# Optimization experiments

Hardware: AMD Instinct MI355X
Metric: run time of the kernel (lower is better)

The kernel has to match this reference:

```python
import jax, jax.numpy as jnp
import numpy as np

B, S, D = 4, 2048, 512      # batch, seq_len, input_dim
E, H = 512, 8               # embed_dim, n_heads
HD = E // H                 # head_dim
ALPHA = 1.0                 # LRSA temperature


def setup_inputs() -> dict:
    key = jax.random.key(0)
    kx, kw1, kw2 = jax.random.split(key, 3)
    # xavier_uniform bounds for the two Linear layers (bias init is 0, as in module)
    b_qkv = float(np.sqrt(6.0 / (D + 3 * E)))
    b_o = float(np.sqrt(6.0 / (E + E)))
    return {
        "x": jax.random.normal(kx, (B, S, D), dtype=jnp.float32),
        "Wqkv": jax.random.uniform(kw1, (3 * E, D), jnp.float32, -b_qkv, b_qkv),
        "bqkv": jnp.zeros((3 * E,), jnp.float32),
        "Wo": jax.random.uniform(kw2, (E, E), jnp.float32, -b_o, b_o),
        "bo": jnp.zeros((E,), jnp.float32),
    }


def reference(x, Wqkv, bqkv, Wo, bo):
    Bx, Sx, _ = x.shape
    # QKV projection: [B,S,3E] -> [B,S,H,3*HD] -> [B,H,S,3*HD]
    qkv = (x @ Wqkv.T + bqkv).reshape(Bx, Sx, H, 3 * HD).transpose(0, 2, 1, 3)
    q, k, v = jnp.split(qkv, 3, axis=-1)  # each [B,H,S,HD]

    # LRSA: pairwise squared L2 distance logits ||q_i - k_j||^2
    q_norm2 = jnp.sum(q * q, axis=-1, keepdims=True)        # [B,H,S,1]
    k_norm2 = jnp.sum(k * k, axis=-1)[..., None, :]         # [B,H,1,S]
    qk = jnp.einsum("bhqd,bhkd->bhqk", q, k)                # [B,H,S,S]
    logits = q_norm2 - 2.0 * qk + k_norm2

    # global normalizers: frobenius norm of q, max per-token L2 norm of x
    fro_q = jnp.sqrt(jnp.sum(q * q))
    inf_2_x = jnp.max(jnp.sqrt(jnp.sum(x * x, axis=-1)))
    logits = logits / fro_q / inf_2_x

    attention = jax.nn.softmax(-ALPHA * logits, axis=-1)    # [B,H,S,S]
    values = jnp.einsum("bhqk,bhkd->bhqd", attention, v)    # [B,H,S,HD]
    values = values.transpose(0, 2, 1, 3).reshape(Bx, Sx, E)
    return values @ Wo.T + bo
```

## Files before the change

kernel.cpp:

```cpp
#include <hip/hip_runtime.h>
#include <hip/hip_bf16.h>
#include <math.h>

#define B_ 4
#define S_ 2048
#define D_ 512
#define E_ 512
#define H_ 8
#define HD_ 64
#define ALPHA_ 1.0f
#define M_ (B_*S_)
#define LOG2E_ 1.44269504088896340736f

typedef __attribute__((ext_vector_type(8))) short bf16x8;
typedef __attribute__((ext_vector_type(4))) float f32x4;

__device__ inline unsigned short f2bf(float f) {
    union { __hip_bfloat16 h; unsigned short u; } cv;
    cv.h = __float2bfloat16(f);
    return cv.u;
}
__device__ inline unsigned pack2bf(float a, float b) {
    union { __hip_bfloat162 h; unsigned u; } cv;
    cv.h = __float22bfloat162_rn(make_float2(a, b));
    return cv.u;
}

__global__ __launch_bounds__(256) void prep(const float* __restrict__ x,
                                            const float* __restrict__ Wqkv,
                                            const float* __restrict__ Wo,
                                            unsigned short* __restrict__ xbf,
                                            unsigned short* __restrict__ Wqkvb,
                                            unsigned short* __restrict__ Wob,
                                            float* __restrict__ xmax) {
    const int t   = threadIdx.x;
    const int bid = blockIdx.x;
    if (bid < 2048) {
        __shared__ float red[4];
        const int wid = t >> 6, lane = t & 63;
        const int row = bid * 4 + wid;
        const float* xr = &x[(size_t)row * D_ + lane * 8];
        const float4 a = *(const float4*)xr;
        const float4 b = *(const float4*)(xr + 4);
        float ss = a.x*a.x + a.y*a.y + a.z*a.z + a.w*a.w
                 + b.x*b.x + b.y*b.y + b.z*b.z + b.w*b.w;
        uint4 o;
        o.x = pack2bf(a.x, a.y); o.y = pack2bf(a.z, a.w);
        o.z = pack2bf(b.x, b.y); o.w = pack2bf(b.z, b.w);
        *(uint4*)&xbf[(size_t)row * D_ + lane * 8] = o;
        #pragma unroll
        for (int off = 32; off; off >>= 1) ss += __shfl_xor(ss, off);
        if (lane == 0) red[wid] = ss;
        __syncthreads();
        if (t == 0)
            xmax[bid] = fmaxf(fmaxf(red[0], red[1]), fmaxf(red[2], red[3]));
    } else {
        const int i  = (bid - 2048) * 256 + t;
        const int nq = 3 * E_ * D_ / 8;
        const float* src; unsigned short* dst; int j;
        if (i < nq) { src = Wqkv; dst = Wqkvb; j = i; }
        else        { src = Wo;   dst = Wob;   j = i - nq; }
        const float4 a = *(const float4*)&src[(size_t)j * 8];
        const float4 b = *(const float4*)&src[(size_t)j * 8 + 4];
        uint4 o;
        o.x = pack2bf(a.x, a.y); o.y = pack2bf(a.z, a.w);
        o.z = pack2bf(b.x, b.y); o.w = pack2bf(b.z, b.w);
        *(uint4*)&dst[(size_t)j * 8] = o;
    }
}

template<int N, int MODE>
__global__ __launch_bounds__(256) void gemm_mfma(const unsigned short* __restrict__ Abf,
                                                 const unsigned short* __restrict__ Wbf,
                                                 const float* __restrict__ bias,
                                                 void* __restrict__ out0,
                                                 void* __restrict__ out1,
                                                 void* __restrict__ out2,
                                                 float* __restrict__ part,
                                                 float* __restrict__ kn2) {
    __shared__ __align__(16) char At[16384];
    __shared__ __align__(16) char Wt[16384];

    const int t  = threadIdx.x;
    const int w  = t >> 6;
    const int l  = t & 63;
    const int g  = l >> 4;
    const int c  = l & 15;
    const int wm = w >> 1;
    const int wn = w & 1;
    const int m0 = blockIdx.y * 128;
    const int n0 = blockIdx.x * 128;

    f32x4 acc[4][4];
    #pragma unroll
    for (int i = 0; i < 4; ++i)
        #pragma unroll
        for (int j = 0; j < 4; ++j)
            #pragma unroll
            for (int r = 0; r < 4; ++r) acc[i][j][r] = 0.f;

    for (int k0 = 0; k0 < 512; k0 += 64) {
        __syncthreads();
        #pragma unroll
        for (int i = 0; i < 4; ++i) {
            const int idx = t + i * 256;
            const int r   = idx >> 3;
            const int j   = idx & 7;
            const int dst = r * 128 + ((j * 16) ^ ((r & 7) << 4));
            *(uint4*)(At + dst) = *(const uint4*)&Abf[(size_t)(m0 + r) * 512 + k0 + j * 8];
            *(uint4*)(Wt + dst) = *(const uint4*)&Wbf[(size_t)(n0 + r) * 512 + k0 + j * 8];
        }
        __syncthreads();

        bf16x8 af[4][2], wf[4][2];
        #pragma unroll
        for (int mt = 0; mt < 4; ++mt) {
            const int row = wm * 64 + mt * 16 + c;
            const int sw  = (row & 7) << 4;
            #pragma unroll
            for (int kc = 0; kc < 2; ++kc)
                af[mt][kc] = *(const bf16x8*)(At + row * 128 + (((kc * 4 + g) * 16) ^ sw));
        }
        #pragma unroll
        for (int nt = 0; nt < 4; ++nt) {
            const int row = wn * 64 + nt * 16 + c;
            const int sw  = (row & 7) << 4;
            #pragma unroll
            for (int kc = 0; kc < 2; ++kc)
                wf[nt][kc] = *(const bf16x8*)(Wt + row * 128 + (((kc * 4 + g) * 16) ^ sw));
        }
        #pragma unroll
        for (int mt = 0; mt < 4; ++mt)
            #pragma unroll
            for (int nt = 0; nt < 4; ++nt) {
                acc[mt][nt] = __builtin_amdgcn_mfma_f32_16x16x32_bf16(af[mt][0], wf[nt][0], acc[mt][nt], 0, 0, 0);
                acc[mt][nt] = __builtin_amdgcn_mfma_f32_16x16x32_bf16(af[mt][1], wf[nt][1], acc[mt][nt], 0, 0, 0);
            }
    }

    if (MODE == 1) {
        #pragma unroll
        for (int mt = 0; mt < 4; ++mt)
            #pragma unroll
            for (int reg = 0; reg < 4; ++reg) {
                const int m = m0 + wm * 64 + mt * 16 + g * 4 + reg;
                #pragma unroll
                for (int nt = 0; nt < 4; ++nt) {
                    const int n = n0 + wn * 64 + nt * 16 + c;
                    ((float*)out0)[(size_t)m * N + n] = acc[mt][nt][reg] + bias[n];
                }
            }
        return;
    }

    const int hb  = 2 * blockIdx.x + wn;
    const int cls = hb % 3;
    const int h   = hb / 3;
    const int b   = m0 >> 11;
    const int s0w = (m0 & 2047) + wm * 64;
    const size_t bhS = ((size_t)b * H_ + h) * S_;

    float kp[4][4];
    #pragma unroll
    for (int i = 0; i < 4; ++i)
        #pragma unroll
        for (int j = 0; j < 4; ++j) kp[i][j] = 0.f;

    if (cls == 2) {
        unsigned short* Vt_ = (unsigned short*)out2;
        #pragma unroll
        for (int nt = 0; nt < 4; ++nt) {
            const int n = n0 + wn * 64 + nt * 16 + c;
            const float bv = bias[n];
            const int d = nt * 16 + c;
            unsigned short* dbase = Vt_ + (((size_t)b * H_ + h) * HD_ + d) * S_ + s0w;
            #pragma unroll
            for (int mt = 0; mt < 4; ++mt) {
                uint2 pk;
                pk.x = pack2bf(acc[mt][nt][0] + bv, acc[mt][nt][1] + bv);
                pk.y = pack2bf(acc[mt][nt][2] + bv, acc[mt][nt][3] + bv);
                *(uint2*)&dbase[mt * 16 + g * 4] = pk;
            }
        }
    } else {
        unsigned short* dst0 = (cls == 0) ? (unsigned short*)out0 : (unsigned short*)out1;
        #pragma unroll
        for (int nt = 0; nt < 4; ++nt) {
            const int n = n0 + wn * 64 + nt * 16 + c;
            const float bv = bias[n];
            const int d = nt * 16 + c;
            #pragma unroll
            for (int mt = 0; mt < 4; ++mt)
                #pragma unroll
                for (int reg = 0; reg < 4; ++reg) {
                    const int s = s0w + mt * 16 + g * 4 + reg;
                    const float val = acc[mt][nt][reg] + bv;
                    kp[mt][reg] = fmaf(val, val, kp[mt][reg]);
                    dst0[(bhS + s) * HD_ + d] = f2bf(val);
                }
        }
    }

    __syncthreads();
    if (cls == 1) {
        float* scratch = (float*)At + wm * 1088;
        #pragma unroll
        for (int i = 0; i < 16; ++i) scratch[l * 17 + i] = kp[i >> 2][i & 3];
        asm volatile("s_waitcnt lgkmcnt(0)" ::: "memory");
        __builtin_amdgcn_sched_barrier(0);
        float sum = 0.f;
        #pragma unroll
        for (int cc = 0; cc < 16; ++cc)
            sum += scratch[(g * 16 + cc) * 17 + c];
        const int s = s0w + (c >> 2) * 16 + g * 4 + (c & 3);
        kn2[bhS + s] = sum;
    }
    __syncthreads();

    float qss = 0.f;
    if (cls == 0) {
        #pragma unroll
        for (int i = 0; i < 4; ++i)
            #pragma unroll
            for (int j = 0; j < 4; ++j) qss += kp[i][j];
    }
    float* red = (float*)At;
    red[t] = qss;
    __syncthreads();
    for (int s = 128; s; s >>= 1) {
        if (t < s) red[t] += red[t + s];
        __syncthreads();
    }
    if (t == 0) part[blockIdx.y * gridDim.x + blockIdx.x] = red[0];
}

__global__ __launch_bounds__(256) void finalize_scale(const float* __restrict__ part,
                                                      const float* __restrict__ xmax,
                                                      float* __restrict__ scal) {
    __shared__ float rs[256], rm[256];
    const int t = threadIdx.x;
    float ss = 0.f, mx = 0.f;
    for (int i = t; i < 768; i += 256) ss += part[i];
    for (int i = t; i < 2048; i += 256) mx = fmaxf(mx, xmax[i]);
    rs[t] = ss; rm[t] = mx;
    __syncthreads();
    for (int s = 128; s; s >>= 1) {
        if (t < s) { rs[t] += rs[t + s]; rm[t] = fmaxf(rm[t], rm[t + s]); }
        __syncthreads();
    }
    if (t == 0) scal[0] = ALPHA_ * LOG2E_ / (sqrtf(rs[0]) * sqrtf(rm[0]));
}

__global__ __launch_bounds__(512) void attn_mfma(const unsigned short* __restrict__ Qb,
                                                 const unsigned short* __restrict__ Kb,
                                                 const unsigned short* __restrict__ Vtb,
                                                 const float* __restrict__ KN2,
                                                 const float* __restrict__ scal,
                                                 unsigned short* __restrict__ VALS) {
    __shared__ __align__(16) char lds[24832];
    char* Kt  = lds;
    char* Vt  = lds + 8192;
    char* Pex = lds + 16384;
    float* kn2s = (float*)(lds + 24576);

    const int t  = threadIdx.x;
    const int w  = t >> 6;
    const int l  = t & 63;
    const int g  = l >> 4;
    const int c  = l & 15;
    const int bid  = blockIdx.y * gridDim.x + blockIdx.x;
    const int swid = (bid & 7) * 64 + (bid >> 3);
    const int bh = swid >> 4;
    const int qb = swid & 15;
    const float sc    = scal[0];
    const float ts2   = 2.0f * sc;
    const float nscal = -sc;

    const int qrow = qb * 128 + w * 16 + c;
    const size_t qoff = ((size_t)bh * S_ + qrow) * HD_;
    const bf16x8 qf0 = *(const bf16x8*)&Qb[qoff + g * 8];
    const bf16x8 qf1 = *(const bf16x8*)&Qb[qoff + 32 + g * 8];

    f32x4 acc[4];
    #pragma unroll
    for (int dt = 0; dt < 4; ++dt)
        #pragma unroll
        for (int r = 0; r < 4; ++r) acc[dt][r] = 0.f;
    float lpart = 0.f;

    const size_t kbase  = (size_t)bh * S_ * HD_;
    const size_t vtbase = (size_t)bh * HD_ * S_;
    const float* kn2g = &KN2[(size_t)bh * S_];
    char* Pw = (w < 4) ? (Kt + w * 2048) : (Pex + (w - 4) * 2048);
    const int swc = (c & 7) << 4;

    const int rr = t >> 3;
    const int jj = (t & 7) * 8;
    const size_t koff0 = kbase + (size_t)rr * HD_ + jj;
    const size_t voff0 = vtbase + (size_t)rr * S_ + jj;
    const int d0 = rr * 128 + ((jj * 2) ^ ((rr & 7) << 4));

    uint4 kA, vA, kB, vB;
    float nA, nB;

#define LOADT(K0, V0, NN, off) do {                                           \
        K0 = *(const uint4*)&Kb[koff0 + (size_t)(off) * HD_];                 \
        V0 = *(const uint4*)&Vtb[voff0 + (off)];                              \
        NN = (t < 64) ? (nscal * kn2g[(off) + t]) : 0.f;                      \
    } while (0)

#define STORET(K0, V0, NN) do {                                               \
        *(uint4*)(Kt + d0) = K0;                                              \
        *(uint4*)(Vt + d0) = V0;                                              \
        if (t < 64) kn2s[t] = NN;                                             \
    } while (0)

    auto compute_tile = [&]() {
        float sl[16];
        #pragma unroll
        for (int kt = 0; kt < 4; ++kt) {
            const int r  = kt * 16 + c;
            const int sw = (r & 7) << 4;
            const bf16x8 ka0 = *(const bf16x8*)(Kt + r * 128 + ((g * 16) ^ sw));
            const bf16x8 ka1 = *(const bf16x8*)(Kt + r * 128 + ((64 + g * 16) ^ sw));
            f32x4 sacc = {0.f, 0.f, 0.f, 0.f};
            sacc = __builtin_amdgcn_mfma_f32_16x16x32_bf16(ka0, qf0, sacc, 0, 0, 0);
            sacc = __builtin_amdgcn_mfma_f32_16x16x32_bf16(ka1, qf1, sacc, 0, 0, 0);
            const f32x4 kn4 = *(const f32x4*)&kn2s[kt * 16 + g * 4];
            #pragma unroll
            for (int rg = 0; rg < 4; ++rg)
                sl[kt * 4 + rg] = fmaf(sacc[rg], ts2, kn4[rg]);
        }
        __syncthreads();

        float p[16];
        #pragma unroll
        for (int j = 0; j < 16; ++j) { p[j] = exp2f(sl[j]); lpart += p[j]; }

        #pragma unroll
        for (int kt = 0; kt < 4; ++kt) {
            uint2 pk;
            pk.x = pack2bf(p[kt * 4 + 0], p[kt * 4 + 1]);
            pk.y = pack2bf(p[kt * 4 + 2], p[kt * 4 + 3]);
            const int cb = kt * 32 + g * 8;
            *(uint2*)(Pw + c * 128 + (cb ^ swc)) = pk;
        }
        asm volatile("s_waitcnt lgkmcnt(0)" ::: "memory");
        __builtin_amdgcn_sched_barrier(0);

        const bf16x8 pa0 = *(const bf16x8*)(Pw + c * 128 + ((g * 16) ^ swc));
        const bf16x8 pa1 = *(const bf16x8*)(Pw + c * 128 + ((64 + g * 16) ^ swc));
        #pragma unroll
        for (int dt = 0; dt < 4; ++dt) {
            const int r  = dt * 16 + c;
            const int sw = (r & 7) << 4;
            const bf16x8 vb0 = *(const bf16x8*)(Vt + r * 128 + ((g * 16) ^ sw));
            const bf16x8 vb1 = *(const bf16x8*)(Vt + r * 128 + ((64 + g * 16) ^ sw));
            acc[dt] = __builtin_amdgcn_mfma_f32_16x16x32_bf16(pa0, vb0, acc[dt], 0, 0, 0);
            acc[dt] = __builtin_amdgcn_mfma_f32_16x16x32_bf16(pa1, vb1, acc[dt], 0, 0, 0);
        }
    };

    LOADT(kA, vA, nA, 0);
    for (int kt0 = 0; kt0 < S_; kt0 += 128) {
        __syncthreads();
        STORET(kA, vA, nA);
        __syncthreads();
        LOADT(kB, vB, nB, kt0 + 64);
        compute_tile();
        __syncthreads();
        STORET(kB, vB, nB);
        __syncthreads();
        if (kt0 + 128 < S_) LOADT(kA, vA, nA, kt0 + 128);
        compute_tile();
    }
#undef LOADT
#undef STORET

    lpart += __shfl_xor(lpart, 16);
    lpart += __shfl_xor(lpart, 32);

    const int b = bh >> 3, h = bh & 7;
    #pragma unroll
    for (int reg = 0; reg < 4; ++reg) {
        const float lq  = __shfl(lpart, g * 4 + reg);
        const float inv = 1.0f / lq;
        const int qg = qb * 128 + w * 16 + g * 4 + reg;
        unsigned short* dst = &VALS[((size_t)b * S_ + qg) * E_ + h * HD_];
        #pragma unroll
        for (int dt = 0; dt < 4; ++dt)
            dst[dt * 16 + c] = f2bf(acc[dt][reg] * inv);
    }
}

extern "C" void kernel_launch(void* const* d_in, const int* in_sizes, int n_in,
                              void* d_out, int out_size, void* d_ws, size_t ws_size,
                              hipStream_t stream) {
    const float* x    = (const float*)d_in[0];
    const float* Wqkv = (const float*)d_in[1];
    const float* bqkv = (const float*)d_in[2];
    const float* Wo   = (const float*)d_in[3];
    const float* bo   = (const float*)d_in[4];
    float* out = (float*)d_out;

    char* ws = (char*)d_ws;
    unsigned short* Qb    = (unsigned short*)(ws);
    unsigned short* Kb    = (unsigned short*)(ws + ((size_t) 8 << 20));
    unsigned short* Vtb   = (unsigned short*)(ws + ((size_t)16 << 20));
    unsigned short* VALb  = (unsigned short*)(ws + ((size_t)24 << 20));
    unsigned short* xbf   = (unsigned short*)(ws + ((size_t)32 << 20));
    unsigned short* Wqkvb = (unsigned short*)(ws + ((size_t)40 << 20));
    unsigned short* Wob   = (unsigned short*)(ws + ((size_t)42 << 20));
    float* KN2  = (float*)(ws + ((size_t)43 << 20));
    float* PART = (float*)(ws + ((size_t)43 << 20) + (256 << 10));
    float* XMAX = (float*)(ws + ((size_t)43 << 20) + (260 << 10));
    float* SCAL = (float*)(ws + ((size_t)43 << 20) + (272 << 10));

    prep<<<2560, 256, 0, stream>>>(x, Wqkv, Wo, xbf, Wqkvb, Wob, XMAX);

    gemm_mfma<3 * E_, 0><<<dim3(12, 64), 256, 0, stream>>>(xbf, Wqkvb, bqkv, Qb, Kb, Vtb, PART, KN2);

    finalize_scale<<<1, 256, 0, stream>>>(PART, XMAX, SCAL);

    attn_mfma<<<dim3(16, 32), 512, 0, stream>>>(Qb, Kb, Vtb, KN2, SCAL, VALb);

    gemm_mfma<E_, 1><<<dim3(4, 64), 256, 0, stream>>>(VALb, Wob, bo, out, nullptr, nullptr, nullptr, nullptr);
}
```

Baseline: 127.0 us.

## Switch attention to 32x32x16 MFMA with register-resident P via lane shuffles

```diff
diff --git a/kernel.cpp b/kernel.cpp
--- a/kernel.cpp
+++ b/kernel.cpp
@@ -14,6 +14,7 @@
 
 typedef __attribute__((ext_vector_type(8))) short bf16x8;
 typedef __attribute__((ext_vector_type(4))) float f32x4;
+typedef __attribute__((ext_vector_type(16))) float f32x16;
 
 __device__ inline unsigned short f2bf(float f) {
     union { __hip_bfloat16 h; unsigned short u; } cv;
@@ -251,23 +252,22 @@
     if (t == 0) scal[0] = ALPHA_ * LOG2E_ / (sqrtf(rs[0]) * sqrtf(rm[0]));
 }
 
-__global__ __launch_bounds__(512) void attn_mfma(const unsigned short* __restrict__ Qb,
-                                                 const unsigned short* __restrict__ Kb,
-                                                 const unsigned short* __restrict__ Vtb,
-                                                 const float* __restrict__ KN2,
-                                                 const float* __restrict__ scal,
-                                                 unsigned short* __restrict__ VALS) {
-    __shared__ __align__(16) char lds[24832];
-    char* Kt  = lds;
-    char* Vt  = lds + 8192;
-    char* Pex = lds + 16384;
-    float* kn2s = (float*)(lds + 24576);
-
-    const int t  = threadIdx.x;
-    const int w  = t >> 6;
-    const int l  = t & 63;
-    const int g  = l >> 4;
-    const int c  = l & 15;
+__global__ __launch_bounds__(256, 2) void attn_mfma(const unsigned short* __restrict__ Qb,
+                                                    const unsigned short* __restrict__ Kb,
+                                                    const unsigned short* __restrict__ Vtb,
+                                                    const float* __restrict__ KN2,
+                                                    const float* __restrict__ scal,
+                                                    unsigned short* __restrict__ VALS) {
+    __shared__ __align__(16) char lds[16640];
+    char* Kt = lds;
+    char* Vt = lds + 8192;
+    float* kn2s = (float*)(lds + 16384);
+
+    const int t   = threadIdx.x;
+    const int w   = t >> 6;
+    const int l   = t & 63;
+    const int h   = l >> 5;
+    const int c32 = l & 31;
     const int bid  = blockIdx.y * gridDim.x + blockIdx.x;
     const int swid = (bid & 7) * 64 + (bid >> 3);
     const int bh = swid >> 4;
@@ -276,120 +276,138 @@
     const float ts2   = 2.0f * sc;
     const float nscal = -sc;
 
-    const int qrow = qb * 128 + w * 16 + c;
+    const int qrow = qb * 128 + w * 32 + c32;
     const size_t qoff = ((size_t)bh * S_ + qrow) * HD_;
-    const bf16x8 qf0 = *(const bf16x8*)&Qb[qoff + g * 8];
-    const bf16x8 qf1 = *(const bf16x8*)&Qb[qoff + 32 + g * 8];
-
-    f32x4 acc[4];
-    #pragma unroll
-    for (int dt = 0; dt < 4; ++dt)
-        #pragma unroll
-        for (int r = 0; r < 4; ++r) acc[dt][r] = 0.f;
+    bf16x8 qf[4];
+    #pragma unroll
+    for (int kc = 0; kc < 4; ++kc)
+        qf[kc] = *(const bf16x8*)&Qb[qoff + kc * 16 + h * 8];
+
+    f32x16 oacc0, oacc1;
+    #pragma unroll
+    for (int i = 0; i < 16; ++i) { oacc0[i] = 0.f; oacc1[i] = 0.f; }
     float lpart = 0.f;
 
     const size_t kbase  = (size_t)bh * S_ * HD_;
     const size_t vtbase = (size_t)bh * HD_ * S_;
     const float* kn2g = &KN2[(size_t)bh * S_];
-    char* Pw = (w < 4) ? (Kt + w * 2048) : (Pex + (w - 4) * 2048);
-    const int swc = (c & 7) << 4;
-
-    const int rr = t >> 3;
-    const int jj = (t & 7) * 8;
-    const size_t koff0 = kbase + (size_t)rr * HD_ + jj;
-    const size_t voff0 = vtbase + (size_t)rr * S_ + jj;
-    const int d0 = rr * 128 + ((jj * 2) ^ ((rr & 7) << 4));
-
-    uint4 kA, vA, kB, vB;
+
+    int offF[2][4];
+    #pragma unroll
+    for (int a = 0; a < 2; ++a)
+        #pragma unroll
+        for (int kc = 0; kc < 4; ++kc)
+            offF[a][kc] = (a * 32 + c32) * 128 + ((kc * 32 + h * 16) ^ ((c32 & 7) << 4));
+
+    const int r0 = t >> 3, r1 = (t + 256) >> 3;
+    const int jc0 = (t & 7) * 8, jc1 = jc0;
+    const size_t koffA = kbase + (size_t)r0 * HD_ + jc0;
+    const size_t koffB = kbase + (size_t)r1 * HD_ + jc1;
+    const size_t voffA = vtbase + (size_t)r0 * S_ + jc0;
+    const size_t voffB = vtbase + (size_t)r1 * S_ + jc1;
+    const int dA = r0 * 128 + ((jc0 * 2) ^ ((r0 & 7) << 4));
+    const int dB = r1 * 128 + ((jc1 * 2) ^ ((r1 & 7) << 4));
+
+    uint4 kA0, kA1, vA0, vA1, kB0, kB1, vB0, vB1;
     float nA, nB;
 
-#define LOADT(K0, V0, NN, off) do {                                           \
-        K0 = *(const uint4*)&Kb[koff0 + (size_t)(off) * HD_];                 \
-        V0 = *(const uint4*)&Vtb[voff0 + (off)];                              \
+#define LOADT(K0, K1, V0, V1, NN, off) do {                                   \
+        K0 = *(const uint4*)&Kb[koffA + (size_t)(off) * HD_];                 \
+        K1 = *(const uint4*)&Kb[koffB + (size_t)(off) * HD_];                 \
+        V0 = *(const uint4*)&Vtb[voffA + (off)];                              \
+        V1 = *(const uint4*)&Vtb[voffB + (off)];                              \
         NN = (t < 64) ? (nscal * kn2g[(off) + t]) : 0.f;                      \
     } while (0)
 
-#define STORET(K0, V0, NN) do {                                               \
-        *(uint4*)(Kt + d0) = K0;                                              \
-        *(uint4*)(Vt + d0) = V0;                                              \
+#define STORET(K0, K1, V0, V1, NN) do {                                       \
+        *(uint4*)(Kt + dA) = K0; *(uint4*)(Kt + dB) = K1;                     \
+        *(uint4*)(Vt + dA) = V0; *(uint4*)(Vt + dB) = V1;                     \
         if (t < 64) kn2s[t] = NN;                                             \
     } while (0)
 
     auto compute_tile = [&]() {
-        float sl[16];
-        #pragma unroll
-        for (int kt = 0; kt < 4; ++kt) {
-            const int r  = kt * 16 + c;
-            const int sw = (r & 7) << 4;
-            const bf16x8 ka0 = *(const bf16x8*)(Kt + r * 128 + ((g * 16) ^ sw));
-            const bf16x8 ka1 = *(const bf16x8*)(Kt + r * 128 + ((64 + g * 16) ^ sw));
-            f32x4 sacc = {0.f, 0.f, 0.f, 0.f};
-            sacc = __builtin_amdgcn_mfma_f32_16x16x32_bf16(ka0, qf0, sacc, 0, 0, 0);
-            sacc = __builtin_amdgcn_mfma_f32_16x16x32_bf16(ka1, qf1, sacc, 0, 0, 0);
-            const f32x4 kn4 = *(const f32x4*)&kn2s[kt * 16 + g * 4];
-            #pragma unroll
-            for (int rg = 0; rg < 4; ++rg)
-                sl[kt * 4 + rg] = fmaf(sacc[rg], ts2, kn4[rg]);
-        }
-        __syncthreads();
-
-        float p[16];
-        #pragma unroll
-        for (int j = 0; j < 16; ++j) { p[j] = exp2f(sl[j]); lpart += p[j]; }
-
-        #pragma unroll
-        for (int kt = 0; kt < 4; ++kt) {
-            uint2 pk;
-            pk.x = pack2bf(p[kt * 4 + 0], p[kt * 4 + 1]);
-            pk.y = pack2bf(p[kt * 4 + 2], p[kt * 4 + 3]);
-            const int cb = kt * 32 + g * 8;
-            *(uint2*)(Pw + c * 128 + (cb ^ swc)) = pk;
-        }
-        asm volatile("s_waitcnt lgkmcnt(0)" ::: "memory");
-        __builtin_amdgcn_sched_barrier(0);
-
-        const bf16x8 pa0 = *(const bf16x8*)(Pw + c * 128 + ((g * 16) ^ swc));
-        const bf16x8 pa1 = *(const bf16x8*)(Pw + c * 128 + ((64 + g * 16) ^ swc));
-        #pragma unroll
-        for (int dt = 0; dt < 4; ++dt) {
-            const int r  = dt * 16 + c;
-            const int sw = (r & 7) << 4;
-            const bf16x8 vb0 = *(const bf16x8*)(Vt + r * 128 + ((g * 16) ^ sw));
-            const bf16x8 vb1 = *(const bf16x8*)(Vt + r * 128 + ((64 + g * 16) ^ sw));
-            acc[dt] = __builtin_amdgcn_mfma_f32_16x16x32_bf16(pa0, vb0, acc[dt], 0, 0, 0);
-            acc[dt] = __builtin_amdgcn_mfma_f32_16x16x32_bf16(pa1, vb1, acc[dt], 0, 0, 0);
+        unsigned pk[2][4][2];
+        #pragma unroll
+        for (int kt = 0; kt < 2; ++kt) {
+            f32x16 sacc;
+            #pragma unroll
+            for (int i = 0; i < 16; ++i) sacc[i] = 0.f;
+            #pragma unroll
+            for (int kc = 0; kc < 4; ++kc) {
+                const bf16x8 ka = *(const bf16x8*)(Kt + offF[kt][kc]);
+                sacc = __builtin_amdgcn_mfma_f32_32x32x16_bf16(ka, qf[kc], sacc, 0, 0, 0);
+            }
+            #pragma unroll
+            for (int rg2 = 0; rg2 < 4; ++rg2) {
+                const f32x4 kn = *(const f32x4*)&kn2s[kt * 32 + 4 * h + 8 * rg2];
+                float pv[4];
+                #pragma unroll
+                for (int m = 0; m < 4; ++m) {
+                    const float sl = fmaf(sacc[4 * rg2 + m], ts2, kn[m]);
+                    pv[m] = exp2f(sl);
+                    lpart += pv[m];
+                }
+                pk[kt][rg2][0] = pack2bf(pv[0], pv[1]);
+                pk[kt][rg2][1] = pack2bf(pv[2], pv[3]);
+            }
+        }
+
+        bf16x8 paf[4];
+        #pragma unroll
+        for (int kc = 0; kc < 4; ++kc) {
+            const int tt = kc >> 1;
+            const int bs = (kc & 1) * 2;
+            const unsigned own0 = h ? pk[tt][bs + 1][0] : pk[tt][bs][0];
+            const unsigned own1 = h ? pk[tt][bs + 1][1] : pk[tt][bs][1];
+            const unsigned snd0 = h ? pk[tt][bs][0]     : pk[tt][bs + 1][0];
+            const unsigned snd1 = h ? pk[tt][bs][1]     : pk[tt][bs + 1][1];
+            const unsigned rcv0 = __shfl_xor(snd0, 32);
+            const unsigned rcv1 = __shfl_xor(snd1, 32);
+            union { bf16x8 v; unsigned u[4]; } fr;
+            fr.u[0] = h ? rcv0 : own0;
+            fr.u[1] = h ? rcv1 : own1;
+            fr.u[2] = h ? own0 : rcv0;
+            fr.u[3] = h ? own1 : rcv1;
+            paf[kc] = fr.v;
+        }
+
+        #pragma unroll
+        for (int kc = 0; kc < 4; ++kc) {
+            const bf16x8 vb0 = *(const bf16x8*)(Vt + offF[0][kc]);
+            const bf16x8 vb1 = *(const bf16x8*)(Vt + offF[1][kc]);
+            oacc0 = __builtin_amdgcn_mfma_f32_32x32x16_bf16(paf[kc], vb0, oacc0, 0, 0, 0);
+            oacc1 = __builtin_amdgcn_mfma_f32_32x32x16_bf16(paf[kc], vb1, oacc1, 0, 0, 0);
         }
     };
 
-    LOADT(kA, vA, nA, 0);
+    LOADT(kA0, kA1, vA0, vA1, nA, 0);
     for (int kt0 = 0; kt0 < S_; kt0 += 128) {
         __syncthreads();
-        STORET(kA, vA, nA);
-        __syncthreads();
-        LOADT(kB, vB, nB, kt0 + 64);
+        STORET(kA0, kA1, vA0, vA1, nA);
+        __syncthreads();
+        LOADT(kB0, kB1, vB0, vB1, nB, kt0 + 64);
         compute_tile();
         __syncthreads();
-        STORET(kB, vB, nB);
-        __syncthreads();
-        if (kt0 + 128 < S_) LOADT(kA, vA, nA, kt0 + 128);
+        STORET(kB0, kB1, vB0, vB1, nB);
+        __syncthreads();
+        if (kt0 + 128 < S_) LOADT(kA0, kA1, vA0, vA1, nA, kt0 + 128);
         compute_tile();
     }
 #undef LOADT
 #undef STORET
 
-    lpart += __shfl_xor(lpart, 16);
     lpart += __shfl_xor(lpart, 32);
 
-    const int b = bh >> 3, h = bh & 7;
-    #pragma unroll
-    for (int reg = 0; reg < 4; ++reg) {
-        const float lq  = __shfl(lpart, g * 4 + reg);
+    const int b = bh >> 3, head = bh & 7;
+    #pragma unroll
+    for (int reg = 0; reg < 16; ++reg) {
+        const int q_local = (reg & 3) + 8 * (reg >> 2) + 4 * h;
+        const float lq  = __shfl(lpart, q_local);
         const float inv = 1.0f / lq;
-        const int qg = qb * 128 + w * 16 + g * 4 + reg;
-        unsigned short* dst = &VALS[((size_t)b * S_ + qg) * E_ + h * HD_];
-        #pragma unroll
-        for (int dt = 0; dt < 4; ++dt)
-            dst[dt * 16 + c] = f2bf(acc[dt][reg] * inv);
+        const int s = qb * 128 + w * 32 + q_local;
+        unsigned short* dst = &VALS[((size_t)b * S_ + s) * E_ + head * HD_];
+        dst[c32]      = f2bf(oacc0[reg] * inv);
+        dst[32 + c32] = f2bf(oacc1[reg] * inv);
     }
 }
 
@@ -422,7 +440,7 @@
 
     finalize_scale<<<1, 256, 0, stream>>>(PART, XMAX, SCAL);
 
-    attn_mfma<<<dim3(16, 32), 512, 0, stream>>>(Qb, Kb, Vtb, KN2, SCAL, VALb);
+    attn_mfma<<<dim3(16, 32), 256, 0, stream>>>(Qb, Kb, Vtb, KN2, SCAL, VALb);
 
     gemm_mfma<E_, 1><<<dim3(4, 64), 256, 0, stream>>>(VALb, Wob, bo, out, nullptr, nullptr, nullptr, nullptr);
 }
```

New measurement: 134.4 us. 1.06x slower.
